# Optimization experiments

Hardware: AMD Instinct MI355X
Metric: run time of the kernel (lower is better)

## Reference

```python
import jax, jax.numpy as jnp
import numpy as np

B, S, ENC, DEC, ATTN = 64, 2048, 512, 512, 256

def setup_inputs() -> dict:
    key = jax.random.key(0)
    k1, k2, k3, k4, k5 = jax.random.split(key, 5)
    s = 0.05
    return {
        "enc_outputs": jax.random.normal(k1, (B, S, ENC), dtype=jnp.float32),
        "dec_state": jax.random.normal(k2, (B, DEC), dtype=jnp.float32),
        "W_enc": jax.random.normal(k3, (ENC, ATTN), dtype=jnp.float32) * s,
        "W_dec": jax.random.normal(k4, (DEC, ATTN), dtype=jnp.float32) * s,
        "v": jax.random.normal(k5, (ATTN,), dtype=jnp.float32) * s,
    }

def reference(enc_outputs, dec_state, W_enc, W_dec, v):
    # enc_proj: [B,S,A], dec_proj: [B,1,A]
    enc_proj = jnp.einsum('bse,ea->bsa', enc_outputs, W_enc)
    dec_proj = jnp.einsum('bd,da->ba', dec_state, W_dec)[:, None, :]
    scores = jnp.einsum('bsa,a->bs', jnp.tanh(enc_proj + dec_proj), v)  # [B,S]
    attn_weights = jax.nn.softmax(scores, axis=-1)
    context = jnp.einsum('bs,bse->be', attn_weights, enc_outputs)  # [B,ENC]
    return (context, attn_weights)
```

## Files before the change

kernel.cpp:

```cpp
#include <hip/hip_runtime.h>
#include <hip/hip_bf16.h>
#include <stdint.h>

#define B_    64
#define S_    2048
#define ENC_  512
#define ATTN_ 256

typedef __bf16 bf16;
typedef bf16  bf16x8 __attribute__((ext_vector_type(8)));
typedef float f32x4  __attribute__((ext_vector_type(4)));

__device__ __forceinline__ float fexp2(float x) {
#if __has_builtin(__builtin_amdgcn_exp2f)
    return __builtin_amdgcn_exp2f(x);
#else
    return exp2f(x);
#endif
}
__device__ __forceinline__ float frcp(float x) {
#if __has_builtin(__builtin_amdgcn_rcpf)
    return __builtin_amdgcn_rcpf(x);
#else
    return 1.0f / x;
#endif
}
__device__ __forceinline__ float fast_tanh(float x) {
    float e = fexp2(x * 2.8853900817779268f);
    return 1.0f - 2.0f * frcp(e + 1.0f);
}

__device__ __forceinline__ void async_copy16(const void* g, void* l) {
#if __has_builtin(__builtin_amdgcn_global_load_lds)
    __builtin_amdgcn_global_load_lds(
        (__attribute__((address_space(1))) void*)(g),
        (__attribute__((address_space(3))) void*)(l), 16, 0, 0);
#else
    *(uint4*)l = *(const uint4*)g;
#endif
}

__global__ __launch_bounds__(256) void k_setup(const float* __restrict__ W_enc,
                                               const float* __restrict__ dec_state,
                                               const float* __restrict__ W_dec,
                                               bf16* __restrict__ WT,
                                               float* __restrict__ dp,
                                               float* __restrict__ ctx) {
    int blk = blockIdx.x;
    if (blk < 512) {
        int idx = blk * 256 + threadIdx.x;
        int n = idx >> 9;
        int k = idx & 511;
        WT[idx] = (bf16)W_enc[k * ATTN_ + n];
    } else {
        int b = blk - 512;
        int a = threadIdx.x;
        *(float2*)(ctx + b * 512 + a * 2) = make_float2(0.f, 0.f);
        const float* ds = dec_state + b * 512;
        float acc = 0.f;
#pragma unroll 8
        for (int d = 0; d < 512; ++d)
            acc += ds[d] * W_dec[d * ATTN_ + a];
        dp[b * ATTN_ + a] = acc;
    }
}

__device__ __forceinline__ void stage_b(const bf16* __restrict__ WT, bf16* bsbuf,
                                        int ks, int bcol4, int bslot, int tid) {
#pragma unroll
    for (int r = 0; r < 4; ++r) {
        int c = r * 64 + bcol4;
        int g = bslot ^ ((c + (c >> 2)) & 3);
        async_copy16(WT + (size_t)c * 512 + ks * 32 + g * 8,
                     bsbuf + r * 2048 + tid * 8);
    }
}

__device__ __forceinline__ void load_a4(const float* s, float4& f0, float4& f1,
                                        float4& f2, float4& f3) {
    f0 = *(const float4*)(s);
    f1 = *(const float4*)(s + 4);
    f2 = *(const float4*)(s + 8);
    f3 = *(const float4*)(s + 12);
}

__device__ __forceinline__ void cvt_store(bf16* dst, float4 f0, float4 f1,
                                          float4 f2, float4 f3) {
    bf16x8 lo, hi;
    lo[0]=(bf16)f0.x; lo[1]=(bf16)f0.y; lo[2]=(bf16)f0.z; lo[3]=(bf16)f0.w;
    lo[4]=(bf16)f1.x; lo[5]=(bf16)f1.y; lo[6]=(bf16)f1.z; lo[7]=(bf16)f1.w;
    hi[0]=(bf16)f2.x; hi[1]=(bf16)f2.y; hi[2]=(bf16)f2.z; hi[3]=(bf16)f2.w;
    hi[4]=(bf16)f3.x; hi[5]=(bf16)f3.y; hi[6]=(bf16)f3.z; hi[7]=(bf16)f3.w;
    *(bf16x8*)(dst)     = lo;
    *(bf16x8*)(dst + 8) = hi;
}

__global__ __launch_bounds__(256, 2) void k_scores(
    const float* __restrict__ enc,
    const bf16*  __restrict__ WT,
    const float* __restrict__ dp,
    const float* __restrict__ v,
    float* __restrict__ out_scores)
{
    __shared__ __align__(16) bf16 As[2][128 * 40];
    __shared__ __align__(16) bf16 Bs[2][256 * 32];
    __shared__ float partial[4][64];

    const int tid  = threadIdx.x;
    const int wave = tid >> 6;
    const int lane = tid & 63;
    const int l15  = lane & 15;
    const int q    = lane >> 4;
    const int m0   = blockIdx.x * 128;
    const int b    = blockIdx.x >> 4;

    const int mrow0 = (wave >> 1) * 64;
    const int ncol0 = (wave & 1) * 128;

    const f32x4 zero4 = {0.f, 0.f, 0.f, 0.f};
    f32x4 acc[4][8];
#pragma unroll
    for (int mt = 0; mt < 4; ++mt)
#pragma unroll
        for (int nt = 0; nt < 8; ++nt)
            acc[mt][nt] = zero4;

    const int arow = tid >> 1;
    const int akc  = tid & 1;
    const float* ag = enc + (size_t)(m0 + arow) * 512 + akc * 16;
    const int aoff = arow * 40 + akc * 16;

    const int bcol4 = tid >> 2;
    const int bslot = tid & 3;

    float4 xa0, xa1, xa2, xa3;
    float4 ya0, ya1, ya2, ya3;

    load_a4(ag,      xa0, xa1, xa2, xa3);
    load_a4(ag + 32, ya0, ya1, ya2, ya3);
    stage_b(WT, Bs[0], 0, bcol4, bslot, tid);
    cvt_store(&As[0][aoff], xa0, xa1, xa2, xa3);
    __syncthreads();

#pragma unroll
    for (int ks = 0; ks < 16; ++ks) {
        const int cur = ks & 1;
        const bf16* Asc = As[cur];
        const bf16* Bsc = Bs[cur];

        bf16x8 af[4];
#pragma unroll
        for (int mt = 0; mt < 4; ++mt) {
            int row = mrow0 + mt * 16 + l15;
            af[mt] = *(const bf16x8*)(Asc + row * 40 + q * 8);
        }
        bf16x8 bfr[8];
#pragma unroll
        for (int nt = 0; nt < 8; ++nt) {
            int col = ncol0 + nt * 16 + l15;
            int p = q ^ ((col + (col >> 2)) & 3);
            bfr[nt] = *(const bf16x8*)(Bsc + col * 32 + p * 8);
        }

        if (ks < 15) stage_b(WT, Bs[cur ^ 1], ks + 1, bcol4, bslot, tid);
        if (ks < 14) {
            const float* s = ag + (ks + 2) * 32;
            if ((ks & 1) == 0) load_a4(s, xa0, xa1, xa2, xa3);
            else               load_a4(s, ya0, ya1, ya2, ya3);
        }

#pragma unroll
        for (int mt = 0; mt < 4; ++mt)
#pragma unroll
            for (int nt = 0; nt < 8; ++nt)
                acc[mt][nt] = __builtin_amdgcn_mfma_f32_16x16x32_bf16(af[mt], bfr[nt], acc[mt][nt], 0, 0, 0);

        if (ks < 15) {
            bf16* dst = &As[cur ^ 1][aoff];
            if ((ks & 1) == 0) cvt_store(dst, ya0, ya1, ya2, ya3);
            else               cvt_store(dst, xa0, xa1, xa2, xa3);
        }
        __syncthreads();
    }

    float dpv[8], vv[8];
#pragma unroll
    for (int nt = 0; nt < 8; ++nt) {
        int col = ncol0 + nt * 16 + l15;
        dpv[nt] = dp[b * 256 + col];
        vv[nt]  = v[col];
    }
#pragma unroll
    for (int mt = 0; mt < 4; ++mt) {
#pragma unroll
        for (int r = 0; r < 4; ++r) {
            float s = 0.f;
#pragma unroll
            for (int nt = 0; nt < 8; ++nt)
                s += fast_tanh(acc[mt][nt][r] + dpv[nt]) * vv[nt];
            s += __shfl_xor(s, 1, 16);
            s += __shfl_xor(s, 2, 16);
            s += __shfl_xor(s, 4, 16);
            s += __shfl_xor(s, 8, 16);
            if (l15 == 0)
                partial[wave][mt * 16 + q * 4 + r] = s;
        }
    }
    __syncthreads();
    if (tid < 128) {
        int mw   = tid >> 6;
        int rloc = tid & 63;
        out_scores[m0 + mw * 64 + rloc] =
            partial[mw * 2][rloc] + partial[mw * 2 + 1][rloc];
    }
}

__global__ __launch_bounds__(256) void k_ctx(const float* __restrict__ enc,
                                             const float* __restrict__ scores,
                                             float* __restrict__ attn,
                                             float* __restrict__ ctx) {
    __shared__ float redm[4], reds[4];
    __shared__ float wlds[64];
    __shared__ f32x4 vred[128];

    const int tid  = threadIdx.x;
    const int wave = tid >> 6;
    const int lane = tid & 63;
    const int b    = blockIdx.x >> 5;
    const int slab = blockIdx.x & 31;
    const float* sc = scores + b * 2048;

    const int eq = tid & 127;
    const int sr = tid >> 7;
    const float* eb = enc + ((size_t)b * 2048 + slab * 64) * 512;

    f32x4 ev0[8];
#pragma unroll
    for (int j = 0; j < 8; ++j)
        ev0[j] = *(const f32x4*)(eb + (size_t)(sr * 8 + j) * 512 + eq * 4);

    float x[8];
    float mx = -1e30f;
#pragma unroll
    for (int i = 0; i < 8; ++i) { x[i] = sc[tid + 256 * i]; mx = fmaxf(mx, x[i]); }
#pragma unroll
    for (int d = 1; d < 64; d <<= 1) mx = fmaxf(mx, __shfl_xor(mx, d));
    if (lane == 0) redm[wave] = mx;
    __syncthreads();
    mx = fmaxf(fmaxf(redm[0], redm[1]), fmaxf(redm[2], redm[3]));

    float e[8];
    float lsum = 0.f;
#pragma unroll
    for (int i = 0; i < 8; ++i) { e[i] = fexp2((x[i] - mx) * 1.4426950408889634f); lsum += e[i]; }
#pragma unroll
    for (int d = 1; d < 64; d <<= 1) lsum += __shfl_xor(lsum, d);
    if (lane == 0) reds[wave] = lsum;
    __syncthreads();
    float inv = 1.0f / (reds[0] + reds[1] + reds[2] + reds[3]);

#pragma unroll
    for (int i = 0; i < 8; ++i) {
        int idx = tid + 256 * i;
        int r   = idx - slab * 64;
        if ((unsigned)r < 64u) {
            float w = e[i] * inv;
            attn[b * 2048 + idx] = w;
            wlds[r] = w;
        }
    }
    __syncthreads();

    f32x4 acc = {0.f, 0.f, 0.f, 0.f};
#pragma unroll
    for (int j = 0; j < 8; ++j) acc += ev0[j] * wlds[sr * 8 + j];

    for (int g = 1; g < 4; ++g) {
        const int sbase = g * 16 + sr * 8;
        f32x4 ev[8];
        float wv[8];
#pragma unroll
        for (int j = 0; j < 8; ++j) {
            ev[j] = *(const f32x4*)(eb + (size_t)(sbase + j) * 512 + eq * 4);
            wv[j] = wlds[sbase + j];
        }
#pragma unroll
        for (int j = 0; j < 8; ++j) acc += ev[j] * wv[j];
    }
    if (sr) vred[eq] = acc;
    __syncthreads();
    if (!sr) {
        acc += vred[eq];
        float* cp = ctx + b * 512 + eq * 4;
        atomicAdd(cp + 0, acc[0]);
        atomicAdd(cp + 1, acc[1]);
        atomicAdd(cp + 2, acc[2]);
        atomicAdd(cp + 3, acc[3]);
    }
}

extern "C" void kernel_launch(void* const* d_in, const int* in_sizes, int n_in,
                              void* d_out, int out_size, void* d_ws, size_t ws_size,
                              hipStream_t stream) {
    const float* enc       = (const float*)d_in[0];
    const float* dec_state = (const float*)d_in[1];
    const float* W_enc     = (const float*)d_in[2];
    const float* W_dec     = (const float*)d_in[3];
    const float* v         = (const float*)d_in[4];

    float* ctx  = (float*)d_out;
    float* attn = (float*)d_out + 64 * 512;

    char*  ws     = (char*)d_ws;
    bf16*  WT     = (bf16*)ws;
    float* dp     = (float*)(ws + 256 * 1024);
    float* scores = (float*)(ws + 256 * 1024 + 64 * 1024);

    k_setup <<<576, 256, 0, stream>>>(W_enc, dec_state, W_dec, WT, dp, ctx);
    k_scores<<<1024, 256, 0, stream>>>(enc, WT, dp, v, scores);
    k_ctx   <<<2048, 256, 0, stream>>>(enc, scores, attn, ctx);
}
```

Before: 449.2 us.

## Fuse context accumulation into scores kernel using unnormalized softmax

```diff
diff --git a/kernel.cpp b/kernel.cpp
--- a/kernel.cpp
+++ b/kernel.cpp
@@ -45,7 +45,8 @@
                                                const float* __restrict__ W_dec,
                                                bf16* __restrict__ WT,
                                                float* __restrict__ dp,
-                                               float* __restrict__ ctx) {
+                                               float* __restrict__ ctx_acc,
+                                               float* __restrict__ esum) {
     int blk = blockIdx.x;
     if (blk < 512) {
         int idx = blk * 256 + threadIdx.x;
@@ -55,7 +56,8 @@
     } else {
         int b = blk - 512;
         int a = threadIdx.x;
-        *(float2*)(ctx + b * 512 + a * 2) = make_float2(0.f, 0.f);
+        *(float2*)(ctx_acc + b * 512 + a * 2) = make_float2(0.f, 0.f);
+        if (a == 0) esum[b] = 0.f;
         const float* ds = dec_state + b * 512;
         float acc = 0.f;
 #pragma unroll 8
@@ -95,16 +97,19 @@
     *(bf16x8*)(dst + 8) = hi;
 }
 
-__global__ __launch_bounds__(256, 2) void k_scores(
+__global__ __launch_bounds__(256, 2) void k_scores_ctx(
     const float* __restrict__ enc,
     const bf16*  __restrict__ WT,
     const float* __restrict__ dp,
     const float* __restrict__ v,
-    float* __restrict__ out_scores)
+    float* __restrict__ attn_e,
+    float* __restrict__ ctx_acc,
+    float* __restrict__ esum)
 {
     __shared__ __align__(16) bf16 As[2][128 * 40];
     __shared__ __align__(16) bf16 Bs[2][256 * 32];
     __shared__ float partial[4][64];
+    __shared__ float ew[128];
 
     const int tid  = threadIdx.x;
     const int wave = tid >> 6;
@@ -207,96 +212,58 @@
         }
     }
     __syncthreads();
+
     if (tid < 128) {
-        int mw   = tid >> 6;
-        int rloc = tid & 63;
-        out_scores[m0 + mw * 64 + rloc] =
-            partial[mw * 2][rloc] + partial[mw * 2 + 1][rloc];
-    }
-}
-
-__global__ __launch_bounds__(256) void k_ctx(const float* __restrict__ enc,
-                                             const float* __restrict__ scores,
-                                             float* __restrict__ attn,
-                                             float* __restrict__ ctx) {
-    __shared__ float redm[4], reds[4];
-    __shared__ float wlds[64];
-    __shared__ f32x4 vred[128];
-
-    const int tid  = threadIdx.x;
-    const int wave = tid >> 6;
-    const int lane = tid & 63;
-    const int b    = blockIdx.x >> 5;
-    const int slab = blockIdx.x & 31;
-    const float* sc = scores + b * 2048;
-
-    const int eq = tid & 127;
-    const int sr = tid >> 7;
-    const float* eb = enc + ((size_t)b * 2048 + slab * 64) * 512;
-
-    f32x4 ev0[8];
-#pragma unroll
-    for (int j = 0; j < 8; ++j)
-        ev0[j] = *(const f32x4*)(eb + (size_t)(sr * 8 + j) * 512 + eq * 4);
-
-    float x[8];
-    float mx = -1e30f;
-#pragma unroll
-    for (int i = 0; i < 8; ++i) { x[i] = sc[tid + 256 * i]; mx = fmaxf(mx, x[i]); }
-#pragma unroll
-    for (int d = 1; d < 64; d <<= 1) mx = fmaxf(mx, __shfl_xor(mx, d));
-    if (lane == 0) redm[wave] = mx;
+        float s = partial[(tid >> 6) * 2][tid & 63] + partial[(tid >> 6) * 2 + 1][tid & 63];
+        float e = fexp2(s * 1.4426950408889634f);
+        ew[tid] = e;
+        attn_e[(size_t)b * 2048 + (blockIdx.x & 15) * 128 + tid] = e;
+        float es = e;
+#pragma unroll
+        for (int d = 1; d < 64; d <<= 1) es += __shfl_xor(es, d);
+        if ((tid & 63) == 0) atomicAdd(esum + b, es);
+    }
     __syncthreads();
-    mx = fmaxf(fmaxf(redm[0], redm[1]), fmaxf(redm[2], redm[3]));
-
-    float e[8];
-    float lsum = 0.f;
-#pragma unroll
-    for (int i = 0; i < 8; ++i) { e[i] = fexp2((x[i] - mx) * 1.4426950408889634f); lsum += e[i]; }
-#pragma unroll
-    for (int d = 1; d < 64; d <<= 1) lsum += __shfl_xor(lsum, d);
-    if (lane == 0) reds[wave] = lsum;
-    __syncthreads();
-    float inv = 1.0f / (reds[0] + reds[1] + reds[2] + reds[3]);
-
-#pragma unroll
-    for (int i = 0; i < 8; ++i) {
-        int idx = tid + 256 * i;
-        int r   = idx - slab * 64;
-        if ((unsigned)r < 64u) {
-            float w = e[i] * inv;
-            attn[b * 2048 + idx] = w;
-            wlds[r] = w;
-        }
-    }
-    __syncthreads();
-
-    f32x4 acc = {0.f, 0.f, 0.f, 0.f};
-#pragma unroll
-    for (int j = 0; j < 8; ++j) acc += ev0[j] * wlds[sr * 8 + j];
-
-    for (int g = 1; g < 4; ++g) {
-        const int sbase = g * 16 + sr * 8;
-        f32x4 ev[8];
-        float wv[8];
-#pragma unroll
-        for (int j = 0; j < 8; ++j) {
-            ev[j] = *(const f32x4*)(eb + (size_t)(sbase + j) * 512 + eq * 4);
-            wv[j] = wlds[sbase + j];
-        }
-#pragma unroll
-        for (int j = 0; j < 8; ++j) acc += ev[j] * wv[j];
-    }
-    if (sr) vred[eq] = acc;
-    __syncthreads();
-    if (!sr) {
-        acc += vred[eq];
-        float* cp = ctx + b * 512 + eq * 4;
-        atomicAdd(cp + 0, acc[0]);
-        atomicAdd(cp + 1, acc[1]);
-        atomicAdd(cp + 2, acc[2]);
-        atomicAdd(cp + 3, acc[3]);
-    }
+
+    {
+        const float* eb = enc + (size_t)m0 * 512;
+        const int col = tid * 2;
+        float cx = 0.f, cy = 0.f;
+#pragma unroll
+        for (int g = 0; g < 16; ++g) {
+            float2 ev[8];
+            float  wv[8];
+#pragma unroll
+            for (int j = 0; j < 8; ++j) {
+                ev[j] = *(const float2*)(eb + (size_t)(g * 8 + j) * 512 + col);
+                wv[j] = ew[g * 8 + j];
+            }
+#pragma unroll
+            for (int j = 0; j < 8; ++j) { cx += ev[j].x * wv[j]; cy += ev[j].y * wv[j]; }
+        }
+        float* cp = ctx_acc + (size_t)b * 512 + col;
+        atomicAdd(cp + 0, cx);
+        atomicAdd(cp + 1, cy);
+    }
+}
+
+__global__ __launch_bounds__(256) void k_finalize(const float* __restrict__ ctx_acc,
+                                                  const float* __restrict__ esum,
+                                                  float* __restrict__ ctx,
+                                                  float* __restrict__ attn) {
+    const int b   = blockIdx.x;
+    const int tid = threadIdx.x;
+    const float inv = 1.0f / esum[b];
+
+    float4* ap = (float4*)(attn + (size_t)b * 2048);
+#pragma unroll
+    for (int i = 0; i < 2; ++i) {
+        float4 t = ap[tid + 256 * i];
+        t.x *= inv; t.y *= inv; t.z *= inv; t.w *= inv;
+        ap[tid + 256 * i] = t;
+    }
+    float2 c = *(const float2*)(ctx_acc + (size_t)b * 512 + tid * 2);
+    *(float2*)(ctx + (size_t)b * 512 + tid * 2) = make_float2(c.x * inv, c.y * inv);
 }
 
 extern "C" void kernel_launch(void* const* d_in, const int* in_sizes, int n_in,
@@ -311,12 +278,13 @@
     float* ctx  = (float*)d_out;
     float* attn = (float*)d_out + 64 * 512;
 
-    char*  ws     = (char*)d_ws;
-    bf16*  WT     = (bf16*)ws;
-    float* dp     = (float*)(ws + 256 * 1024);
-    float* scores = (float*)(ws + 256 * 1024 + 64 * 1024);
-
-    k_setup <<<576, 256, 0, stream>>>(W_enc, dec_state, W_dec, WT, dp, ctx);
-    k_scores<<<1024, 256, 0, stream>>>(enc, WT, dp, v, scores);
-    k_ctx   <<<2048, 256, 0, stream>>>(enc, scores, attn, ctx);
-}
+    char*  ws      = (char*)d_ws;
+    bf16*  WT      = (bf16*)ws;
+    float* dp      = (float*)(ws + 256 * 1024);
+    float* ctx_acc = (float*)(ws + 256 * 1024 + 64 * 1024);
+    float* esum    = (float*)(ws + 256 * 1024 + 64 * 1024 + 128 * 1024);
+
+    k_setup      <<<576,  256, 0, stream>>>(W_enc, dec_state, W_dec, WT, dp, ctx_acc, esum);
+    k_scores_ctx <<<1024, 256, 0, stream>>>(enc, WT, dp, v, attn, ctx_acc, esum);
+    k_finalize   <<<64,   256, 0, stream>>>(ctx_acc, esum, ctx, attn);
+}
```

Result: faster. 437.6 us (-2.6%).
